# Kernel optimization log

Measured on AMD Instinct MI355X. Metric: run time of the kernel, lower is better.

## Reference

```python
import jax, jax.numpy as jnp
import numpy as np


def setup_inputs() -> dict:
    key = jax.random.key(0)
    ks = jax.random.split(key, 7)
    B, C, H, W = 8, 256, 64, 64
    Cp = C // 8
    sc = 1.0 / np.sqrt(C)
    return {
        "x": jax.random.normal(ks[0], (B, C, H, W), dtype=jnp.float32),
        "Wq": jax.random.normal(ks[1], (Cp, C), dtype=jnp.float32) * sc,
        "bq": jnp.zeros((Cp,), dtype=jnp.float32),
        "Wk": jax.random.normal(ks[2], (Cp, C), dtype=jnp.float32) * sc,
        "bk": jnp.zeros((Cp,), dtype=jnp.float32),
        "Wv": jax.random.normal(ks[3], (C, C), dtype=jnp.float32) * sc,
        "bv": jnp.zeros((C,), dtype=jnp.float32),
        "gamma": jnp.float32(0.5),
    }


def reference(x, Wq, bq, Wk, bk, Wv, bv, gamma):
    B, C, H, W = x.shape
    xf = x.reshape(B, C, H * W)                         # (B, C, N)
    # 1x1 Conv1d == per-position linear over channels
    q = jnp.einsum('dc,bcn->bnd', Wq, xf) + bq          # (B, N, Cp)
    k = jnp.einsum('dc,bcn->bdn', Wk, xf) + bk[:, None] # (B, Cp, N)
    v = jnp.einsum('dc,bcn->bdn', Wv, xf) + bv[:, None] # (B, C, N)
    scores = jnp.einsum('bnd,bdm->bnm', q, k)           # (B, N, N)
    attn = jax.nn.softmax(scores, axis=-1)              # (B, N, N)
    # o = v @ attn^T : o[:, :, n] = sum_m attn[n, m] * v[:, :, m]
    o = jnp.einsum('bcm,bnm->bcn', v, attn)             # (B, C, N)
    o = o.reshape(B, C, H, W)
    return gamma * o + x
```

## Files before the change

kernel.cpp:

```cpp
#include <hip/hip_runtime.h>
#include <hip/hip_bf16.h>


constexpr int C  = 256;
constexpr int CP = 32;
constexpr int NPOS = 4096;
constexpr int NB = 8;
constexpr int MT = 64;
constexpr int NT = NPOS / MT;
constexpr float LOG2E = 1.44269504088896340736f;

typedef __attribute__((ext_vector_type(4))) float  f32x4;
typedef __attribute__((ext_vector_type(4))) short  bf16x4;
typedef __attribute__((ext_vector_type(8))) short  bf16x8;

__device__ __forceinline__ void bar_lds() {
    asm volatile("s_waitcnt lgkmcnt(0)\n\ts_barrier" ::: "memory");
}
__device__ __forceinline__ void wait_vm0() {
    asm volatile("s_waitcnt vmcnt(0)" ::: "memory");
}
__device__ __forceinline__ void wait_vm4() {
    asm volatile("s_waitcnt vmcnt(4)" ::: "memory");
}
__device__ __forceinline__ void wait_vm1() {
    asm volatile("s_waitcnt vmcnt(1)" ::: "memory");
}
__device__ __forceinline__ void gl_lds16(const void* gsrc, void* ldst) {
    typedef const __attribute__((address_space(1))) void* gp_t;
    typedef __attribute__((address_space(3))) void* lp_t;
    __builtin_amdgcn_global_load_lds((gp_t)gsrc, (lp_t)ldst, 16, 0, 0);
}
__device__ __forceinline__ short f2bf(float f) {
    __hip_bfloat16 h = __float2bfloat16(f);
    return __builtin_bit_cast(short, h);
}
__device__ __forceinline__ float ex2(float f) {
    return __builtin_amdgcn_exp2f(f);
}
__device__ __forceinline__ f32x4 mfma16(bf16x8 a, bf16x8 b, f32x4 c) {
    return __builtin_amdgcn_mfma_f32_16x16x32_bf16(a, b, c, 0, 0, 0);
}

__global__ __launch_bounds__(256) void wprep_kernel(
    const float* __restrict__ Wq, const float* __restrict__ bq,
    const float* __restrict__ Wk, const float* __restrict__ bk,
    const float* __restrict__ Wv, const float* __restrict__ bv,
    __hip_bfloat16* __restrict__ wh, __hip_bfloat16* __restrict__ wl,
    float* __restrict__ bcat)
{
    const int r = blockIdx.x, c = threadIdx.x;
    float w;
    if (r < 32)      w = Wq[r * 256 + c];
    else if (r < 64) w = Wk[(r - 32) * 256 + c];
    else             w = Wv[(r - 64) * 256 + c];
    __hip_bfloat16 h = __float2bfloat16(w);
    wh[r * 256 + c] = h;
    wl[r * 256 + c] = __float2bfloat16(w - __bfloat162float(h));
    if (c == 0)
        bcat[r] = (r < 32) ? bq[r] : (r < 64) ? bk[r - 32] : bv[r - 64];
}

__global__ __launch_bounds__(256) void xtrans_kernel(
    const float* __restrict__ x, __hip_bfloat16* __restrict__ xT)
{
    __shared__ float xl[64][65];
    const int tid = threadIdx.x;
    const int b   = blockIdx.x >> 8;
    const int rem = blockIdx.x & 255;
    const int c0  = (rem >> 6) << 6;
    const int n0  = (rem & 63) << 6;

    const float* xb = x + ((size_t)b * C + c0) * NPOS + n0;
    #pragma unroll
    for (int k = 0; k < 4; ++k) {
        const int idx = tid + k * 256;
        const int c = idx >> 4, j4 = idx & 15;
        float4 gg = *reinterpret_cast<const float4*>(xb + (size_t)c * NPOS + j4 * 4);
        xl[c][j4 * 4 + 0] = gg.x; xl[c][j4 * 4 + 1] = gg.y;
        xl[c][j4 * 4 + 2] = gg.z; xl[c][j4 * 4 + 3] = gg.w;
    }
    __syncthreads();

    const int nl = tid >> 2, cseg = tid & 3;
    bf16x8 o0, o1;
    #pragma unroll
    for (int j = 0; j < 8; ++j) {
        o0[j] = f2bf(xl[cseg * 16 + j][nl]);
        o1[j] = f2bf(xl[cseg * 16 + 8 + j][nl]);
    }
    __hip_bfloat16* dst = xT + ((size_t)b * NPOS + n0 + nl) * C + c0 + cseg * 16;
    *reinterpret_cast<bf16x8*>(dst)     = o0;
    *reinterpret_cast<bf16x8*>(dst + 8) = o1;
}

__global__ __launch_bounds__(512)
__attribute__((amdgpu_waves_per_eu(4)))
void qkv_mfma_kernel(
    const __hip_bfloat16* __restrict__ xT,
    const __hip_bfloat16* __restrict__ wh, const __hip_bfloat16* __restrict__ wl,
    const float* __restrict__ bcat,
    __hip_bfloat16* __restrict__ qh, __hip_bfloat16* __restrict__ ql,
    __hip_bfloat16* __restrict__ kh, __hip_bfloat16* __restrict__ kl,
    __hip_bfloat16* __restrict__ vT)
{
    __shared__ __align__(16) __hip_bfloat16 xlds[16384];
    __shared__ __align__(16) __hip_bfloat16 wlds[3][4096];

    const int tid = threadIdx.x;
    const int b  = blockIdx.x & 7;
    const int n0 = (blockIdx.x >> 3) << 6;
    const int l  = tid & 63;
    const int g  = tid >> 6;
    const int G  = l >> 4;
    const int li = l & 15;
    const int cs = g >> 1, ns0 = (g & 1) * 2;

    #pragma unroll
    for (int j = 0; j < 4; ++j)
        gl_lds16(xT + ((size_t)b * NPOS + n0 + l) * C + (j * 8 + g) * 8,
                 xlds + (j * 512 + g * 64) * 8);

    auto stageW = [&](int t, int d) {
        const int ct = t >> 3, ks = t & 7;
        const __hip_bfloat16* src = (g < 4) ? wh : wl;
        const int gg = g & 3;
        gl_lds16(src + (size_t)(ct * 64 + l) * 256 + ks * 32 + gg * 8,
                 &wlds[d][((g >= 4) ? 2048 : 0) + gg * 512]);
    };
    stageW(0, 0);
    stageW(1, 1);

    f32x4 acc0 = (f32x4){0.f, 0.f, 0.f, 0.f};
    f32x4 acc1 = (f32x4){0.f, 0.f, 0.f, 0.f};

    for (int t = 0; t < 40; ++t) {
        wait_vm1();
        bar_lds();
        if (t + 2 < 40) stageW(t + 2, (t + 2) % 3);

        const int ks = t & 7;
        const __hip_bfloat16* wb = wlds[t % 3];
        bf16x8 whf = *reinterpret_cast<const bf16x8*>(wb + (G * 64 + cs * 16 + li) * 8);
        bf16x8 wlf = *reinterpret_cast<const bf16x8*>(wb + 2048 + (G * 64 + cs * 16 + li) * 8);
        bf16x8 xf0 = *reinterpret_cast<const bf16x8*>(
            xlds + (ks * 256 + G * 64 + ns0 * 16 + li) * 8);
        bf16x8 xf1 = *reinterpret_cast<const bf16x8*>(
            xlds + (ks * 256 + G * 64 + (ns0 + 1) * 16 + li) * 8);
        acc0 = mfma16(whf, xf0, acc0);
        acc0 = mfma16(wlf, xf0, acc0);
        acc1 = mfma16(whf, xf1, acc1);
        acc1 = mfma16(wlf, xf1, acc1);

        if (ks == 7) {
            const int ct = t >> 3;
            const int cb = ct * 64 + cs * 16 + G * 4;
            const float4 b4 = *reinterpret_cast<const float4*>(bcat + cb);
            const float bb[4] = {b4.x, b4.y, b4.z, b4.w};
            #pragma unroll
            for (int j = 0; j < 2; ++j) {
                const f32x4 a = j ? acc1 : acc0;
                const int n_abs = n0 + (ns0 + j) * 16 + li;
                if (ct == 0) {
                    __hip_bfloat16* hb = (cs < 2) ? qh : kh;
                    __hip_bfloat16* lb = (cs < 2) ? ql : kl;
                    const float qsc = (cs < 2) ? LOG2E : 1.0f;
                    const int cq = (cs < 2) ? cb : cb - 32;
                    const size_t base = ((size_t)b * NPOS + n_abs) * CP + cq;
                    #pragma unroll
                    for (int r = 0; r < 4; ++r) {
                        const float val = (a[r] + bb[r]) * qsc;
                        __hip_bfloat16 h = __float2bfloat16(val);
                        hb[base + r] = h;
                        lb[base + r] = __float2bfloat16(val - __bfloat162float(h));
                    }
                } else {
                    const int cv = cb - 64;
                    #pragma unroll
                    for (int r = 0; r < 4; ++r)
                        vT[((size_t)b * C + cv + r) * NPOS + n_abs] =
                            __float2bfloat16(a[r] + bb[r]);
                }
            }
            acc0 = (f32x4){0.f, 0.f, 0.f, 0.f};
            acc1 = (f32x4){0.f, 0.f, 0.f, 0.f};
        }
    }
}

__global__ __launch_bounds__(512)
__attribute__((amdgpu_waves_per_eu(4)))
void attn_kernel(
    const __hip_bfloat16* __restrict__ qh, const __hip_bfloat16* __restrict__ ql,
    const __hip_bfloat16* __restrict__ kh, const __hip_bfloat16* __restrict__ kl,
    const __hip_bfloat16* __restrict__ vT, const float* __restrict__ x,
    const float* __restrict__ gamma_p, float* __restrict__ out)
{
    __shared__ __align__(16) __hip_bfloat16 k_lds[2][2][2048];
    __shared__ __align__(16) __hip_bfloat16 p_lds[2][64][64];
    __shared__ float psm[2][64];

    const int tid = threadIdx.x;
    const int b  = blockIdx.x & 7;
    const int qt = blockIdx.x >> 3;
    const int l  = tid & 63;
    const int g  = tid >> 6;
    const int G  = l >> 4;
    const int li = l & 15;
    const int nj = g & 3, gr = g >> 2;
    const int mi0 = gr * 2;
    const int sn = nj * 16 + li;
    const int swz = (li & 7) << 4;

    const __hip_bfloat16* khb = kh + (size_t)b * NPOS * CP;
    const __hip_bfloat16* klb = kl + (size_t)b * NPOS * CP;
    const __hip_bfloat16* vTb = vT + (size_t)b * C * NPOS;

    bf16x8 qhf, qlf;
    {
        const size_t qoff = ((size_t)b * NPOS + qt * 64 + nj * 16 + li) * CP + G * 8;
        qhf = *reinterpret_cast<const bf16x8*>(qh + qoff);
        qlf = *reinterpret_cast<const bf16x8*>(ql + qoff);
    }

    const __hip_bfloat16* vp0 = vTb + (size_t)(g * 32 + li) * NPOS + G * 8;
    const __hip_bfloat16* vp1 = vTb + (size_t)(g * 32 + 16 + li) * NPOS + G * 8;

    f32x4 acc[4][2];
    #pragma unroll
    for (int nt = 0; nt < 4; ++nt)
        #pragma unroll
        for (int ct = 0; ct < 2; ++ct) acc[nt][ct] = (f32x4){0.f, 0.f, 0.f, 0.f};
    float lsum_reg = 0.f;

    auto stageK = [&](int tt, int bufd) {
        const __hip_bfloat16* ks = (gr == 0) ? khb : klb;
        gl_lds16(ks + (size_t)tt * MT * CP + l * CP + nj * 8,
                 &k_lds[bufd][gr][nj * 512]);
    };
    auto qkp = [&](int PB) {
        const int kfo = (G * 64 + mi0 * 16 + li) * 8;
        bf16x8 kh0 = *reinterpret_cast<const bf16x8*>(&k_lds[PB][0][kfo]);
        bf16x8 kl0 = *reinterpret_cast<const bf16x8*>(&k_lds[PB][1][kfo]);
        bf16x8 kh1 = *reinterpret_cast<const bf16x8*>(&k_lds[PB][0][kfo + 128]);
        bf16x8 kl1 = *reinterpret_cast<const bf16x8*>(&k_lds[PB][1][kfo + 128]);
        f32x4 s0 = (f32x4){0.f, 0.f, 0.f, 0.f};
        s0 = mfma16(kh0, qhf, s0); s0 = mfma16(kh0, qlf, s0); s0 = mfma16(kl0, qhf, s0);
        f32x4 s1 = (f32x4){0.f, 0.f, 0.f, 0.f};
        s1 = mfma16(kh1, qhf, s1); s1 = mfma16(kh1, qlf, s1); s1 = mfma16(kl1, qhf, s1);
        float p0[4], p1[4];
        #pragma unroll
        for (int r = 0; r < 4; ++r) {
            p0[r] = ex2(s0[r]);
            p1[r] = ex2(s1[r]);
        }
        lsum_reg += ((p0[0] + p0[1]) + (p0[2] + p0[3]))
                  + ((p1[0] + p1[1]) + (p1[2] + p1[3]));
        char* prow = reinterpret_cast<char*>(&p_lds[PB][0][0]) + sn * 128;
        bf16x4 w0 = { f2bf(p0[0]), f2bf(p0[1]), f2bf(p0[2]), f2bf(p0[3]) };
        *reinterpret_cast<bf16x4*>(prow + ((gr * 64 + G * 8) ^ swz)) = w0;
        bf16x4 w1 = { f2bf(p1[0]), f2bf(p1[1]), f2bf(p1[2]), f2bf(p1[3]) };
        *reinterpret_cast<bf16x4*>(prow + ((gr * 64 + 32 + G * 8) ^ swz)) = w1;
    };
    auto pv = [&](int PB, const bf16x8 vf[4]) {
        const char* pb = reinterpret_cast<const char*>(&p_lds[PB][0][0]);
        #pragma unroll
        for (int s = 0; s < 2; ++s) {
            const bf16x8 af0 = vf[s];
            const bf16x8 af1 = vf[2 + s];
            #pragma unroll
            for (int nt = 0; nt < 4; ++nt) {
                const bf16x8 bfr = *reinterpret_cast<const bf16x8*>(
                    pb + (nt * 16 + li) * 128 + ((s * 64 + G * 16) ^ swz));
                acc[nt][0] = mfma16(af0, bfr, acc[nt][0]);
                acc[nt][1] = mfma16(af1, bfr, acc[nt][1]);
            }
        }
    };
    auto loadV = [&](bf16x8 vf[4], int tt) {
        const __hip_bfloat16* q0 = vp0 + tt * MT;
        const __hip_bfloat16* q1 = vp1 + tt * MT;
        vf[0] = *reinterpret_cast<const bf16x8*>(q0);
        vf[1] = *reinterpret_cast<const bf16x8*>(q0 + 32);
        vf[2] = *reinterpret_cast<const bf16x8*>(q1);
        vf[3] = *reinterpret_cast<const bf16x8*>(q1 + 32);
    };

    bf16x8 vA[4], vB[4];

    stageK(0, 0);
    stageK(1, 1);
    loadV(vA, 0);
    wait_vm0();
    bar_lds();
    qkp(0);
    bar_lds();

    #pragma unroll 1
    for (int tp = 0; tp < 31; ++tp) {
        const int t = tp * 2;
        stageK(t + 2, 0);
        __builtin_amdgcn_sched_barrier(0);
        loadV(vB, t + 1);
        __builtin_amdgcn_sched_barrier(0);
        __builtin_amdgcn_s_setprio(1);
        qkp(1);
        pv(0, vA);
        __builtin_amdgcn_s_setprio(0);
        wait_vm4();
        bar_lds();
        stageK(t + 3, 1);
        __builtin_amdgcn_sched_barrier(0);
        loadV(vA, t + 2);
        __builtin_amdgcn_sched_barrier(0);
        __builtin_amdgcn_s_setprio(1);
        qkp(0);
        pv(1, vB);
        __builtin_amdgcn_s_setprio(0);
        wait_vm4();
        bar_lds();
    }
    stageK(0, 0);
    __builtin_amdgcn_sched_barrier(0);
    loadV(vB, 63);
    __builtin_amdgcn_sched_barrier(0);
    __builtin_amdgcn_s_setprio(1);
    qkp(1);
    pv(0, vA);
    __builtin_amdgcn_s_setprio(0);
    wait_vm4();
    bar_lds();
    pv(1, vB);

    float ps = lsum_reg;
    ps += __shfl_xor(ps, 16);
    ps += __shfl_xor(ps, 32);
    if (G == 0) psm[gr][sn] = ps;
    bar_lds();

    const float gamma = *gamma_p;
    const float* xb = x   + (size_t)b * C * NPOS;
    float*       ob = out + (size_t)b * C * NPOS;

    #pragma unroll
    for (int nt = 0; nt < 4; ++nt) {
        const int cidx = nt * 16 + li;
        const float inv = 1.0f / (psm[0][cidx] + psm[1][cidx]);
        const int n = qt * 64 + cidx;
        #pragma unroll
        for (int ct = 0; ct < 2; ++ct) {
            const int c0 = g * 32 + ct * 16 + G * 4;
            #pragma unroll
            for (int r = 0; r < 4; ++r) {
                const size_t idx = (size_t)(c0 + r) * NPOS + n;
                ob[idx] = gamma * acc[nt][ct][r] * inv + xb[idx];
            }
        }
    }
}

extern "C" void kernel_launch(void* const* d_in, const int* in_sizes, int n_in,
                              void* d_out, int out_size, void* d_ws, size_t ws_size,
                              hipStream_t stream) {
    const float* x  = (const float*)d_in[0];
    const float* Wq = (const float*)d_in[1];
    const float* bq = (const float*)d_in[2];
    const float* Wk = (const float*)d_in[3];
    const float* bk = (const float*)d_in[4];
    const float* Wv = (const float*)d_in[5];
    const float* bv = (const float*)d_in[6];
    const float* gamma = (const float*)d_in[7];
    float* out = (float*)d_out;

    const size_t qk_n = (size_t)NB * NPOS * CP;
    const size_t v_n  = (size_t)NB * C * NPOS;
    __hip_bfloat16* qhb = (__hip_bfloat16*)d_ws;
    __hip_bfloat16* qlb = qhb + qk_n;
    __hip_bfloat16* khb = qlb + qk_n;
    __hip_bfloat16* klb = khb + qk_n;
    __hip_bfloat16* vT  = klb + qk_n;
    __hip_bfloat16* xT  = vT + v_n;
    __hip_bfloat16* wh  = xT + v_n;
    __hip_bfloat16* wl  = wh + 320 * 256;
    float*          bcat = (float*)(wl + 320 * 256);

    xtrans_kernel<<<NB * 4 * 64, 256, 0, stream>>>(x, xT);
    wprep_kernel<<<320, 256, 0, stream>>>(Wq, bq, Wk, bk, Wv, bv, wh, wl, bcat);
    qkv_mfma_kernel<<<NB * (NPOS / 64), 512, 0, stream>>>(xT, wh, wl, bcat,
                                                          qhb, qlb, khb, klb, vT);
    attn_kernel<<<NB * (NPOS / 64), 512, 0, stream>>>(qhb, qlb, khb, klb, vT,
                                                      x, gamma, out);
}
```

Baseline: 185.4 us.

## Split attention blocks across channel halves with 256-thread blocks

The attention kernel now launches twice as many 256-thread blocks, and each block handles one half of the output channels for a 64-query tile. Each wave computes a 2x2 tile of QK scores and writes its own P slice. Smaller blocks can raise occupancy and shorten barrier waits. In exchange, the QK^T products and softmax exponentials are computed twice per query tile, once per channel half, and K is loaded twice.

Result: slower. 294.9 us (+59.1%).

```diff
diff --git a/kernel.cpp b/kernel.cpp
--- a/kernel.cpp
+++ b/kernel.cpp
@@ -188,7 +188,7 @@
     }
 }
 
-__global__ __launch_bounds__(512)
+__global__ __launch_bounds__(256)
 __attribute__((amdgpu_waves_per_eu(4)))
 void attn_kernel(
     const __hip_bfloat16* __restrict__ qh, const __hip_bfloat16* __restrict__ ql,
@@ -201,66 +201,74 @@
     __shared__ float psm[2][64];
 
     const int tid = threadIdx.x;
-    const int b  = blockIdx.x & 7;
-    const int qt = blockIdx.x >> 3;
+    const int b    = blockIdx.x & 7;
+    const int rest = blockIdx.x >> 3;
+    const int qt   = rest >> 1;
+    const int cs   = rest & 1;
     const int l  = tid & 63;
-    const int g  = tid >> 6;
+    const int w  = tid >> 6;
     const int G  = l >> 4;
     const int li = l & 15;
-    const int nj = g & 3, gr = g >> 2;
-    const int mi0 = gr * 2;
-    const int sn = nj * 16 + li;
+    const int mi = w >> 1, ni2 = w & 1;
     const int swz = (li & 7) << 4;
 
     const __hip_bfloat16* khb = kh + (size_t)b * NPOS * CP;
     const __hip_bfloat16* klb = kl + (size_t)b * NPOS * CP;
     const __hip_bfloat16* vTb = vT + (size_t)b * C * NPOS;
 
-    bf16x8 qhf, qlf;
-    {
-        const size_t qoff = ((size_t)b * NPOS + qt * 64 + nj * 16 + li) * CP + G * 8;
-        qhf = *reinterpret_cast<const bf16x8*>(qh + qoff);
-        qlf = *reinterpret_cast<const bf16x8*>(ql + qoff);
-    }
-
-    const __hip_bfloat16* vp0 = vTb + (size_t)(g * 32 + li) * NPOS + G * 8;
-    const __hip_bfloat16* vp1 = vTb + (size_t)(g * 32 + 16 + li) * NPOS + G * 8;
+    bf16x8 qhf2[2], qlf2[2];
+    #pragma unroll
+    for (int nt2 = 0; nt2 < 2; ++nt2) {
+        const size_t qoff =
+            ((size_t)b * NPOS + qt * 64 + ni2 * 32 + nt2 * 16 + li) * CP + G * 8;
+        qhf2[nt2] = *reinterpret_cast<const bf16x8*>(qh + qoff);
+        qlf2[nt2] = *reinterpret_cast<const bf16x8*>(ql + qoff);
+    }
+
+    const int c0w = cs * 128 + w * 32;
+    const __hip_bfloat16* vp0 = vTb + (size_t)(c0w + li) * NPOS + G * 8;
+    const __hip_bfloat16* vp1 = vTb + (size_t)(c0w + 16 + li) * NPOS + G * 8;
 
     f32x4 acc[4][2];
     #pragma unroll
     for (int nt = 0; nt < 4; ++nt)
         #pragma unroll
         for (int ct = 0; ct < 2; ++ct) acc[nt][ct] = (f32x4){0.f, 0.f, 0.f, 0.f};
-    float lsum_reg = 0.f;
+    float lsum0 = 0.f, lsum1 = 0.f;
 
     auto stageK = [&](int tt, int bufd) {
-        const __hip_bfloat16* ks = (gr == 0) ? khb : klb;
-        gl_lds16(ks + (size_t)tt * MT * CP + l * CP + nj * 8,
-                 &k_lds[bufd][gr][nj * 512]);
+        gl_lds16(khb + (size_t)tt * 2048 + l * 32 + w * 8, &k_lds[bufd][0][w * 512]);
+        gl_lds16(klb + (size_t)tt * 2048 + l * 32 + w * 8, &k_lds[bufd][1][w * 512]);
     };
     auto qkp = [&](int PB) {
-        const int kfo = (G * 64 + mi0 * 16 + li) * 8;
-        bf16x8 kh0 = *reinterpret_cast<const bf16x8*>(&k_lds[PB][0][kfo]);
-        bf16x8 kl0 = *reinterpret_cast<const bf16x8*>(&k_lds[PB][1][kfo]);
-        bf16x8 kh1 = *reinterpret_cast<const bf16x8*>(&k_lds[PB][0][kfo + 128]);
-        bf16x8 kl1 = *reinterpret_cast<const bf16x8*>(&k_lds[PB][1][kfo + 128]);
-        f32x4 s0 = (f32x4){0.f, 0.f, 0.f, 0.f};
-        s0 = mfma16(kh0, qhf, s0); s0 = mfma16(kh0, qlf, s0); s0 = mfma16(kl0, qhf, s0);
-        f32x4 s1 = (f32x4){0.f, 0.f, 0.f, 0.f};
-        s1 = mfma16(kh1, qhf, s1); s1 = mfma16(kh1, qlf, s1); s1 = mfma16(kl1, qhf, s1);
-        float p0[4], p1[4];
+        bf16x8 khf[2], klf[2];
         #pragma unroll
-        for (int r = 0; r < 4; ++r) {
-            p0[r] = ex2(s0[r]);
-            p1[r] = ex2(s1[r]);
+        for (int mt = 0; mt < 2; ++mt) {
+            const int kfo = (G * 64 + (mi * 2 + mt) * 16 + li) * 8;
+            khf[mt] = *reinterpret_cast<const bf16x8*>(&k_lds[PB][0][kfo]);
+            klf[mt] = *reinterpret_cast<const bf16x8*>(&k_lds[PB][1][kfo]);
         }
-        lsum_reg += ((p0[0] + p0[1]) + (p0[2] + p0[3]))
-                  + ((p1[0] + p1[1]) + (p1[2] + p1[3]));
-        char* prow = reinterpret_cast<char*>(&p_lds[PB][0][0]) + sn * 128;
-        bf16x4 w0 = { f2bf(p0[0]), f2bf(p0[1]), f2bf(p0[2]), f2bf(p0[3]) };
-        *reinterpret_cast<bf16x4*>(prow + ((gr * 64 + G * 8) ^ swz)) = w0;
-        bf16x4 w1 = { f2bf(p1[0]), f2bf(p1[1]), f2bf(p1[2]), f2bf(p1[3]) };
-        *reinterpret_cast<bf16x4*>(prow + ((gr * 64 + 32 + G * 8) ^ swz)) = w1;
+        #pragma unroll
+        for (int mt = 0; mt < 2; ++mt) {
+            #pragma unroll
+            for (int nt2 = 0; nt2 < 2; ++nt2) {
+                f32x4 u = (f32x4){0.f, 0.f, 0.f, 0.f};
+                u = mfma16(khf[mt], qhf2[nt2], u);
+                u = mfma16(klf[mt], qhf2[nt2], u);
+                f32x4 v = (f32x4){0.f, 0.f, 0.f, 0.f};
+                v = mfma16(khf[mt], qlf2[nt2], v);
+                float p[4];
+                #pragma unroll
+                for (int r = 0; r < 4; ++r) p[r] = ex2(u[r] + v[r]);
+                const float psum = (p[0] + p[1]) + (p[2] + p[3]);
+                if (nt2 == 0) lsum0 += psum; else lsum1 += psum;
+                const int sn = ni2 * 32 + nt2 * 16 + li;
+                char* prow = reinterpret_cast<char*>(&p_lds[PB][0][0]) + sn * 128;
+                bf16x4 wv = { f2bf(p[0]), f2bf(p[1]), f2bf(p[2]), f2bf(p[3]) };
+                *reinterpret_cast<bf16x4*>(
+                    prow + ((mi * 64 + mt * 32 + G * 8) ^ swz)) = wv;
+            }
+        }
     };
     auto pv = [&](int PB, const bf16x8 vf[4]) {
         const char* pb = reinterpret_cast<const char*>(&p_lds[PB][0][0]);
@@ -332,10 +340,14 @@
     bar_lds();
     pv(1, vB);
 
-    float ps = lsum_reg;
-    ps += __shfl_xor(ps, 16);
-    ps += __shfl_xor(ps, 32);
-    if (G == 0) psm[gr][sn] = ps;
+    lsum0 += __shfl_xor(lsum0, 16);
+    lsum0 += __shfl_xor(lsum0, 32);
+    lsum1 += __shfl_xor(lsum1, 16);
+    lsum1 += __shfl_xor(lsum1, 32);
+    if (G == 0) {
+        psm[mi][ni2 * 32 + li]      = lsum0;
+        psm[mi][ni2 * 32 + 16 + li] = lsum1;
+    }
     bar_lds();
 
     const float gamma = *gamma_p;
@@ -349,7 +361,7 @@
         const int n = qt * 64 + cidx;
         #pragma unroll
         for (int ct = 0; ct < 2; ++ct) {
-            const int c0 = g * 32 + ct * 16 + G * 4;
+            const int c0 = c0w + ct * 16 + G * 4;
             #pragma unroll
             for (int r = 0; r < 4; ++r) {
                 const size_t idx = (size_t)(c0 + r) * NPOS + n;
@@ -388,6 +400,6 @@
     wprep_kernel<<<320, 256, 0, stream>>>(Wq, bq, Wk, bk, Wv, bv, wh, wl, bcat);
     qkv_mfma_kernel<<<NB * (NPOS / 64), 512, 0, stream>>>(xT, wh, wl, bcat,
                                                           qhb, qlb, khb, klb, vT);
-    attn_kernel<<<NB * (NPOS / 64), 512, 0, stream>>>(qhb, qlb, khb, klb, vT,
-                                                      x, gamma, out);
-}
+    attn_kernel<<<NB * (NPOS / 64) * 2, 256, 0, stream>>>(qhb, qlb, khb, klb, vT,
+                                                          x, gamma, out);
+}
```

## Halve attention query tile to 32 rows and double grid size

Applied to the files above, without the earlier changes.

Shrinks each attention block's query tile from 64 to 32 positions, launching twice as many blocks, and remaps the 8 waves so each computes one 16x16 score tile (4 key sub-tiles by 2 query sub-tiles). Row sums are now split over four partial slots. The goal is more blocks in flight across the GPU's compute units and fewer accumulator registers per thread. In exchange, every block re-streams all of K and V for half as many queries, which doubles global and L2 traffic for K/V and the per-block staging overhead.

Measured after the change: 308.1 us. 1.66x slower.

```diff
diff --git a/kernel.cpp b/kernel.cpp
--- a/kernel.cpp
+++ b/kernel.cpp
@@ -197,8 +197,8 @@
     const float* __restrict__ gamma_p, float* __restrict__ out)
 {
     __shared__ __align__(16) __hip_bfloat16 k_lds[2][2][2048];
-    __shared__ __align__(16) __hip_bfloat16 p_lds[2][64][64];
-    __shared__ float psm[2][64];
+    __shared__ __align__(16) __hip_bfloat16 p_lds[2][32][64];
+    __shared__ float psm[4][32];
 
     const int tid = threadIdx.x;
     const int b  = blockIdx.x & 7;
@@ -207,8 +207,8 @@
     const int g  = tid >> 6;
     const int G  = l >> 4;
     const int li = l & 15;
-    const int nj = g & 3, gr = g >> 2;
-    const int mi0 = gr * 2;
+    const int mi = g >> 1, nj = g & 1;
+    const int gr = g >> 2, njs = g & 3;
     const int sn = nj * 16 + li;
     const int swz = (li & 7) << 4;
 
@@ -218,7 +218,7 @@
 
     bf16x8 qhf, qlf;
     {
-        const size_t qoff = ((size_t)b * NPOS + qt * 64 + nj * 16 + li) * CP + G * 8;
+        const size_t qoff = ((size_t)b * NPOS + qt * 32 + sn) * CP + G * 8;
         qhf = *reinterpret_cast<const bf16x8*>(qh + qoff);
         qlf = *reinterpret_cast<const bf16x8*>(ql + qoff);
     }
@@ -226,41 +226,31 @@
     const __hip_bfloat16* vp0 = vTb + (size_t)(g * 32 + li) * NPOS + G * 8;
     const __hip_bfloat16* vp1 = vTb + (size_t)(g * 32 + 16 + li) * NPOS + G * 8;
 
-    f32x4 acc[4][2];
-    #pragma unroll
-    for (int nt = 0; nt < 4; ++nt)
+    f32x4 acc[2][2];
+    #pragma unroll
+    for (int nt = 0; nt < 2; ++nt)
         #pragma unroll
         for (int ct = 0; ct < 2; ++ct) acc[nt][ct] = (f32x4){0.f, 0.f, 0.f, 0.f};
     float lsum_reg = 0.f;
 
     auto stageK = [&](int tt, int bufd) {
         const __hip_bfloat16* ks = (gr == 0) ? khb : klb;
-        gl_lds16(ks + (size_t)tt * MT * CP + l * CP + nj * 8,
-                 &k_lds[bufd][gr][nj * 512]);
+        gl_lds16(ks + (size_t)tt * MT * CP + l * CP + njs * 8,
+                 &k_lds[bufd][gr][njs * 512]);
     };
     auto qkp = [&](int PB) {
-        const int kfo = (G * 64 + mi0 * 16 + li) * 8;
+        const int kfo = (G * 64 + mi * 16 + li) * 8;
         bf16x8 kh0 = *reinterpret_cast<const bf16x8*>(&k_lds[PB][0][kfo]);
         bf16x8 kl0 = *reinterpret_cast<const bf16x8*>(&k_lds[PB][1][kfo]);
-        bf16x8 kh1 = *reinterpret_cast<const bf16x8*>(&k_lds[PB][0][kfo + 128]);
-        bf16x8 kl1 = *reinterpret_cast<const bf16x8*>(&k_lds[PB][1][kfo + 128]);
         f32x4 s0 = (f32x4){0.f, 0.f, 0.f, 0.f};
         s0 = mfma16(kh0, qhf, s0); s0 = mfma16(kh0, qlf, s0); s0 = mfma16(kl0, qhf, s0);
-        f32x4 s1 = (f32x4){0.f, 0.f, 0.f, 0.f};
-        s1 = mfma16(kh1, qhf, s1); s1 = mfma16(kh1, qlf, s1); s1 = mfma16(kl1, qhf, s1);
-        float p0[4], p1[4];
+        float p[4];
         #pragma unroll
-        for (int r = 0; r < 4; ++r) {
-            p0[r] = ex2(s0[r]);
-            p1[r] = ex2(s1[r]);
-        }
-        lsum_reg += ((p0[0] + p0[1]) + (p0[2] + p0[3]))
-                  + ((p1[0] + p1[1]) + (p1[2] + p1[3]));
+        for (int r = 0; r < 4; ++r) p[r] = ex2(s0[r]);
+        lsum_reg += (p[0] + p[1]) + (p[2] + p[3]);
         char* prow = reinterpret_cast<char*>(&p_lds[PB][0][0]) + sn * 128;
-        bf16x4 w0 = { f2bf(p0[0]), f2bf(p0[1]), f2bf(p0[2]), f2bf(p0[3]) };
-        *reinterpret_cast<bf16x4*>(prow + ((gr * 64 + G * 8) ^ swz)) = w0;
-        bf16x4 w1 = { f2bf(p1[0]), f2bf(p1[1]), f2bf(p1[2]), f2bf(p1[3]) };
-        *reinterpret_cast<bf16x4*>(prow + ((gr * 64 + 32 + G * 8) ^ swz)) = w1;
+        bf16x4 w0 = { f2bf(p[0]), f2bf(p[1]), f2bf(p[2]), f2bf(p[3]) };
+        *reinterpret_cast<bf16x4*>(prow + ((mi * 32 + G * 8) ^ swz)) = w0;
     };
     auto pv = [&](int PB, const bf16x8 vf[4]) {
         const char* pb = reinterpret_cast<const char*>(&p_lds[PB][0][0]);
@@ -269,7 +259,7 @@
             const bf16x8 af0 = vf[s];
             const bf16x8 af1 = vf[2 + s];
             #pragma unroll
-            for (int nt = 0; nt < 4; ++nt) {
+            for (int nt = 0; nt < 2; ++nt) {
                 const bf16x8 bfr = *reinterpret_cast<const bf16x8*>(
                     pb + (nt * 16 + li) * 128 + ((s * 64 + G * 16) ^ swz));
                 acc[nt][0] = mfma16(af0, bfr, acc[nt][0]);
@@ -332,10 +322,9 @@
     bar_lds();
     pv(1, vB);
 
-    float ps = lsum_reg;
-    ps += __shfl_xor(ps, 16);
-    ps += __shfl_xor(ps, 32);
-    if (G == 0) psm[gr][sn] = ps;
+    lsum_reg += __shfl_xor(lsum_reg, 16);
+    lsum_reg += __shfl_xor(lsum_reg, 32);
+    if (G == 0) psm[mi][sn] = lsum_reg;
     bar_lds();
 
     const float gamma = *gamma_p;
@@ -343,10 +332,11 @@
     float*       ob = out + (size_t)b * C * NPOS;
 
     #pragma unroll
-    for (int nt = 0; nt < 4; ++nt) {
+    for (int nt = 0; nt < 2; ++nt) {
         const int cidx = nt * 16 + li;
-        const float inv = 1.0f / (psm[0][cidx] + psm[1][cidx]);
-        const int n = qt * 64 + cidx;
+        const float inv = 1.0f / (psm[0][cidx] + psm[1][cidx]
+                                + psm[2][cidx] + psm[3][cidx]);
+        const int n = qt * 32 + cidx;
         #pragma unroll
         for (int ct = 0; ct < 2; ++ct) {
             const int c0 = g * 32 + ct * 16 + G * 4;
@@ -388,6 +378,6 @@
     wprep_kernel<<<320, 256, 0, stream>>>(Wq, bq, Wk, bk, Wv, bv, wh, wl, bcat);
     qkv_mfma_kernel<<<NB * (NPOS / 64), 512, 0, stream>>>(xT, wh, wl, bcat,
                                                           qhb, qlb, khb, klb, vT);
-    attn_kernel<<<NB * (NPOS / 64), 512, 0, stream>>>(qhb, qlb, khb, klb, vT,
+    attn_kernel<<<NB * (NPOS / 32), 512, 0, stream>>>(qhb, qlb, khb, klb, vT,
                                                       x, gamma, out);
 }
```
